# Performance work log

Measured on AMD Instinct MI355X. Metric: run time of the kernel, lower is better.

## Reference

```python
import jax, jax.numpy as jnp
import numpy as np

RADIUS = 1.3
COARSE = 32          # coarse_reso
FINE = 2             # fine_reso[0]
NUM_ATOMS = 32
SH_DIM = 9           # (sh_deg+1)^2, sh_deg=2
DATA_DIM = SH_DIM * 3 + 1  # 28
BATCH = 512
N_INT = COARSE * 3 * 2 * FINE  # 384 intersections per ray

# 8 trilinear neighbor offsets, same order as the torch module
_OFFSETS = jnp.array([[-1, -1, -1], [-1, -1, 1], [-1, 1, -1], [-1, 1, 1],
                      [1, -1, -1], [1, -1, 1], [1, 1, -1], [1, 1, 1]], dtype=jnp.float32)


def sh_encode(d):
    """Real spherical harmonics basis, degree 2 (9 components), on normalized dirs."""
    d = d / jnp.linalg.norm(d, axis=-1, keepdims=True)
    x, y, z = d[..., 0], d[..., 1], d[..., 2]
    c0 = 0.28209479177387814
    c1 = 0.48860251190291987
    c2a = 1.0925484305920792
    c2b = 0.31539156525252005
    c2c = 0.5462742152960396
    return jnp.stack([
        c0 * jnp.ones_like(x),
        -c1 * y, c1 * z, -c1 * x,
        c2a * x * y, -c2a * y * z,
        c2b * (2.0 * z * z - x * x - y * y),
        -c2a * x * z,
        c2c * (x * x - y * y)], axis=-1)


def dict_interp(pts, grid, atoms):
    """Multi-res voxel trilinear gather + dictionary-atom accumulate.
    pts: [N,3] world coords; grid: [COARSE^3, A]; atoms: [FINE^3, A, D]."""
    fine_vlen = (2.0 * RADIUS / COARSE) / FINE
    p = (pts + RADIUS) / fine_vlen                       # [N,3] fine-grid coords
    pre = p[:, None, :] + _OFFSETS[None] / 2.0           # [N,8,3]
    post = jnp.clip(jnp.floor(pre), 0.0, COARSE * FINE - 1)
    offs = jnp.abs(p[:, None, :] - (post + 0.5))         # [N,8,3]
    w = jnp.prod(1.0 - offs, axis=-1)                    # [N,8] trilinear weights
    idx = post.astype(jnp.int32)
    c = idx // FINE                                      # coarse cell per-axis
    f = idx % FINE                                       # fine cell per-axis
    cflat = (c[..., 0] * COARSE + c[..., 1]) * COARSE + c[..., 2]  # [N,8]
    fflat = (f[..., 0] * FINE + f[..., 1]) * FINE + f[..., 2]      # [N,8]
    out = jnp.zeros((pts.shape[0], DATA_DIM), pts.dtype)
    for n in range(8):
        cv = grid[cflat[:, n]]                           # [N,A] gathered coarse weights
        av = atoms[fflat[:, n]]                          # [N,A,D] gathered atoms
        out = out + w[:, n, None] * jnp.einsum('na,nad->nd', cv, av)
    return out


def setup_inputs() -> dict:
    key = jax.random.key(0)
    k1, k2, k3, k4 = jax.random.split(key, 4)
    rays_o = jax.random.uniform(k1, (BATCH, 3), jnp.float32, -0.5, 0.5)
    rays_d = jax.random.normal(k2, (BATCH, 3), jnp.float32)
    rays_d = rays_d / jnp.linalg.norm(rays_d, axis=-1, keepdims=True)
    grid = 0.01 * jax.random.normal(k3, (COARSE ** 3, NUM_ATOMS), jnp.float32)
    atoms = jnp.concatenate([
        jax.random.uniform(k4, (FINE ** 3, NUM_ATOMS, DATA_DIM - 1), jnp.float32),
        jnp.full((FINE ** 3, NUM_ATOMS, 1), 0.01, jnp.float32)], axis=-1)
    return {"rays_o": rays_o, "rays_d": rays_d, "grid": grid, "atoms": atoms, "grid_id": 0}


def reference(rays_o, rays_d, grid, atoms, grid_id):
    del grid_id  # single scene
    step = ((2.0 * RADIUS / COARSE) / FINE) / 2.0
    # sample_proposal (no_grad in the original)
    off_pos = (RADIUS - rays_o) / rays_d
    off_neg = (-RADIUS - rays_o) / rays_d
    start = jnp.max(jnp.minimum(off_pos, off_neg), axis=-1, keepdims=True)
    steps = jnp.arange(N_INT, dtype=rays_o.dtype)[None]
    intersections = jax.lax.stop_gradient(start + steps * step)  # [B, N_INT]
    ts = intersections[:, :-1]                                    # [B, S]
    pts = jax.lax.stop_gradient(
        rays_o[:, None, :] + ts[..., None] * rays_d[:, None, :])  # [B,S,3]
    mask = jnp.all((pts > -RADIUS) & (pts < RADIUS), axis=-1)     # [B,S]
    B, S = ts.shape
    data = dict_interp(pts.reshape(-1, 3), grid, atoms).reshape(B, S, DATA_DIM)
    # masked_scatter_ equivalent: zero out out-of-box samples
    sigma = jnp.where(mask, jax.nn.relu(data[..., -1]), 0.0)
    dists = (intersections[:, 1:] - intersections[:, :-1]) * jnp.linalg.norm(rays_d, axis=-1, keepdims=True)
    alpha = 1.0 - jnp.exp(-sigma * dists)
    T = jnp.cumprod(1.0 - alpha + 1e-10, axis=-1)
    T = jnp.concatenate([jnp.ones_like(T[:, :1]), T[:, :-1]], axis=-1)
    abs_light = alpha * T                                         # [B,S]
    sh = sh_encode(rays_d)                                        # [B,SH_DIM]
    sh_vals = data[..., :-1].reshape(B, S, 3, SH_DIM)
    rgb_s = jnp.einsum('bk,bsck->bsc', sh, sh_vals)               # [B,S,3]
    rgb_s = jnp.where(mask[..., None], rgb_s, 0.0)
    rgb = jnp.sum(abs_light[..., None] * jax.nn.sigmoid(rgb_s), axis=1)
    rgb = rgb + (1.0 - jnp.sum(abs_light, axis=-1, keepdims=True))  # white background
    depth = jnp.sum(abs_light * ts, axis=-1)
    consistency_loss = jnp.zeros((), rgb.dtype)  # noise_std == 0
    return rgb, alpha, depth, consistency_loss
```

## Files before the change

### kernel.cpp

```cpp
#include <hip/hip_runtime.h>
#include <math.h>

#define R_ 1.3f
#define NCOARSE 32
#define SAMPLES 383
#define BATCH 512
#define STEPSZ 0.0203125f
#define INV_FINE_VLEN 24.615384615384617f

using f32x4 = __attribute__((ext_vector_type(4))) float;
using s16x8 = __attribute__((ext_vector_type(8))) short;
using u32x4 = __attribute__((ext_vector_type(4))) unsigned int;

__device__ __forceinline__ unsigned int packbf2(float lo, float hi) {
    unsigned int a = __builtin_bit_cast(unsigned int, lo);
    unsigned int b = __builtin_bit_cast(unsigned int, hi);
    a = (a + 0x7fffu + ((a >> 16) & 1u)) >> 16;
    b = (b + 0x7fffu + ((b >> 16) & 1u)) >> 16;
    return (a & 0xffffu) | (b << 16);
}

__device__ __forceinline__ void dimwc(float p, float* W, int* C) {
    float post0 = fminf(fmaxf(floorf(p - 0.5f), 0.f), 63.f);
    float post1 = fminf(fmaxf(floorf(p + 0.5f), 0.f), 63.f);
    float w0 = 1.f - fabsf(p - (post0 + 0.5f));
    float w1 = 1.f - fabsf(p - (post1 + 0.5f));
    int i0 = (int)post0, i1 = (int)post1;
    int f0 = i0 & 1, f1 = i1 & 1;
    W[0] = (f0 == 0 ? w0 : 0.f) + (f1 == 0 ? w1 : 0.f);
    W[1] = (f0 == 1 ? w0 : 0.f) + (f1 == 1 ? w1 : 0.f);
    int c0 = i0 >> 1, c1 = i1 >> 1;
    C[0] = (f0 == 0) ? c0 : c1;
    C[1] = (f0 == 1) ? c0 : c1;
}

__global__ __launch_bounds__(512, 4) void dp_fused(
    const float* __restrict__ rays_o, const float* __restrict__ rays_d,
    const float* __restrict__ grid, const float* __restrict__ atoms,
    float* __restrict__ out_rgb, float* __restrict__ out_alpha,
    float* __restrict__ out_depth, float* __restrict__ out_loss)
{
    __shared__ u32x4 Bf[16][64];
    __shared__ u32x4 Abuf[8][256];
    __shared__ float alpha_l[384];
    __shared__ float sig_l[384][3];

    const int b = blockIdx.x;
    const int tid = threadIdx.x;
    const int wid = tid >> 6, l = tid & 63;
    const int sl = l & 15, fp = l >> 4;
    if (b == 0 && tid == 0) out_loss[0] = 0.f;

    if (tid < 384) alpha_l[tid] = 0.f;
    {
        float* sf = &sig_l[0][0];
        for (int i = tid; i < 384 * 3; i += 512) sf[i] = 0.f;
    }

    for (int sidx = tid; sidx < 1024; sidx += 512) {
        const int ll = sidx & 63, nt = (sidx >> 6) & 1, kb = sidx >> 7;
        const int a0 = (ll >> 4) * 8, d = nt * 16 + (ll & 15);
        u32x4 o = {0u, 0u, 0u, 0u};
        if (d < 28) {
#pragma unroll
            for (int e2 = 0; e2 < 4; ++e2) {
                const float lo = atoms[(kb * 32 + a0 + 2 * e2) * 28 + d];
                const float hi = atoms[(kb * 32 + a0 + 2 * e2 + 1) * 28 + d];
                o[e2] = packbf2(lo, hi);
            }
        }
        Bf[sidx >> 6][ll] = o;
    }

    const float ox = rays_o[3 * b], oy = rays_o[3 * b + 1], oz = rays_o[3 * b + 2];
    const float dx = rays_d[3 * b], dy = rays_d[3 * b + 1], dz = rays_d[3 * b + 2];
    const float start = fmaxf(fmaxf(
        fminf((R_ - ox) / dx, (-R_ - ox) / dx),
        fminf((R_ - oy) / dy, (-R_ - oy) / dy)),
        fminf((R_ - oz) / dz, (-R_ - oz) / dz));
    const float t_exit = fminf(fminf(
        fmaxf((R_ - ox) / dx, (-R_ - ox) / dx),
        fmaxf((R_ - oy) / dy, (-R_ - oy) / dy)),
        fmaxf((R_ - oz) / dz, (-R_ - oz) / dz));
    const int ns = (int)floorf((t_exit - start) / STEPSZ) + 2;
    const int ntiles = min(24, (ns >> 4) + 2);

    const float lend = sqrtf(dx * dx + dy * dy + dz * dz);
    const float dist = STEPSZ * lend;
    const float inv = 1.f / lend;
    const float nx = dx * inv, ny = dy * inv, nz = dz * inv;
    float sh[9];
    sh[0] = 0.28209479177387814f;
    sh[1] = -0.48860251190291987f * ny;
    sh[2] = 0.48860251190291987f * nz;
    sh[3] = -0.48860251190291987f * nx;
    sh[4] = 1.0925484305920792f * nx * ny;
    sh[5] = -1.0925484305920792f * ny * nz;
    sh[6] = 0.31539156525252005f * (2.f * nz * nz - nx * nx - ny * ny);
    sh[7] = -1.0925484305920792f * nx * nz;
    sh[8] = 0.5462742152960396f * (nx * nx - ny * ny);

    __syncthreads();

    u32x4* W4 = &Abuf[wid][0];
    float* Dbuf = (float*)W4;

    for (int t = wid; t < ntiles; t += 8) {
        const int s = t * 16 + sl;
        const float tt = start + s * STEPSZ;
        const float px = ox + tt * dx, py = oy + tt * dy, pz = oz + tt * dz;
        const bool m = (s < SAMPLES) &&
                       (px > -R_ && px < R_ && py > -R_ && py < R_ && pz > -R_ && pz < R_);
        if (__ballot(m) == 0ull) continue;

        float W0[2], W1[2], W2[2];
        int C0[2], C1[2], C2[2];
        dimwc((px + R_) * INV_FINE_VLEN, W0, C0);
        dimwc((py + R_) * INV_FINE_VLEN, W1, C1);
        dimwc((pz + R_) * INV_FINE_VLEN, W2, C2);
        const float msk = m ? 1.f : 0.f;

        f32x4 acc0 = {0.f, 0.f, 0.f, 0.f};
        f32x4 acc1 = {0.f, 0.f, 0.f, 0.f};
#pragma unroll
        for (int stg = 0; stg < 2; ++stg) {
            const int f = 4 * stg + fp;
            const int fx = (f >> 2) & 1, fy = (f >> 1) & 1, fz = f & 1;
            const float wf = msk * W0[fx] * W1[fy] * W2[fz];
            const int cf = (C0[fx] * NCOARSE + C1[fy]) * NCOARSE + C2[fz];
            const f32x4* gr = (const f32x4*)(grid + cf * 32);
#pragma unroll
            for (int g4 = 0; g4 < 4; ++g4) {
                const f32x4 v0 = gr[2 * g4];
                const f32x4 v1 = gr[2 * g4 + 1];
                u32x4 o;
                o.x = packbf2(wf * v0.x, wf * v0.y);
                o.y = packbf2(wf * v0.z, wf * v0.w);
                o.z = packbf2(wf * v1.x, wf * v1.y);
                o.w = packbf2(wf * v1.z, wf * v1.w);
                W4[fp * 64 + 16 * g4 + sl] = o;
            }
#pragma unroll
            for (int kb2 = 0; kb2 < 4; ++kb2) {
                const int kb = 4 * stg + kb2;
                const s16x8 af = __builtin_bit_cast(s16x8, W4[kb2 * 64 + l]);
                acc0 = __builtin_amdgcn_mfma_f32_16x16x32_bf16(
                    af, __builtin_bit_cast(s16x8, Bf[kb * 2 + 0][l]), acc0, 0, 0, 0);
                acc1 = __builtin_amdgcn_mfma_f32_16x16x32_bf16(
                    af, __builtin_bit_cast(s16x8, Bf[kb * 2 + 1][l]), acc1, 0, 0, 0);
            }
        }

#pragma unroll
        for (int r = 0; r < 4; ++r) {
            Dbuf[(4 * fp + r) * 33 + sl]      = acc0[r];
            Dbuf[(4 * fp + r) * 33 + sl + 16] = acc1[r];
        }

        const int s2 = l >> 2, c = l & 3;
        const int so = t * 16 + s2;
        if (c == 3) {
            const float sigma = fmaxf(Dbuf[s2 * 33 + 27], 0.f);
            alpha_l[so] = 1.f - expf(-sigma * dist);
        } else {
            float r_ = 0.f;
#pragma unroll
            for (int k = 0; k < 9; ++k) r_ += sh[k] * Dbuf[s2 * 33 + c * 9 + k];
            sig_l[so][c] = 1.f / (1.f + expf(-r_));
        }
    }

    __syncthreads();

    if (tid < SAMPLES) out_alpha[b * SAMPLES + tid] = alpha_l[tid];

    if (wid == 0) {
        float Tacc = 1.f;
        float r0 = 0.f, r1 = 0.f, r2 = 0.f, sd = 0.f, sa = 0.f;
        for (int j = 0; j < 6; ++j) {
            const int s = j * 64 + l;
            const bool v = s < SAMPLES;
            const float a = v ? alpha_l[s] : 0.f;
            float incl = v ? (1.f - a + 1e-10f) : 1.f;
#pragma unroll
            for (int off = 1; off < 64; off <<= 1) {
                const float tm = __shfl_up(incl, off, 64);
                if (l >= off) incl *= tm;
            }
            float excl = __shfl_up(incl, 1, 64);
            if (l == 0) excl = 1.f;
            const float T = Tacc * excl;
            const float al = a * T;
            if (v) {
                r0 += al * sig_l[s][0];
                r1 += al * sig_l[s][1];
                r2 += al * sig_l[s][2];
                sd += al * (start + s * STEPSZ);
                sa += al;
            }
            Tacc *= __shfl(incl, 63, 64);
        }
#pragma unroll
        for (int m = 32; m > 0; m >>= 1) {
            r0 += __shfl_xor(r0, m, 64);
            r1 += __shfl_xor(r1, m, 64);
            r2 += __shfl_xor(r2, m, 64);
            sd += __shfl_xor(sd, m, 64);
            sa += __shfl_xor(sa, m, 64);
        }
        if (l == 0) {
            const float base = 1.f - sa;
            out_rgb[b * 3 + 0] = r0 + base;
            out_rgb[b * 3 + 1] = r1 + base;
            out_rgb[b * 3 + 2] = r2 + base;
            out_depth[b] = sd;
        }
    }
}

extern "C" void kernel_launch(void* const* d_in, const int* in_sizes, int n_in,
                              void* d_out, int out_size, void* d_ws, size_t ws_size,
                              hipStream_t stream) {
    const float* rays_o = (const float*)d_in[0];
    const float* rays_d = (const float*)d_in[1];
    const float* grid   = (const float*)d_in[2];
    const float* atoms  = (const float*)d_in[3];
    float* out   = (float*)d_out;
    float* rgb   = out;
    float* alpha = out + BATCH * 3;
    float* depth = out + BATCH * 3 + BATCH * SAMPLES;
    float* loss  = out + BATCH * 3 + BATCH * SAMPLES + BATCH;

    dp_fused<<<dim3(BATCH), dim3(512), 0, stream>>>(
        rays_o, rays_d, grid, atoms, rgb, alpha, depth, loss);
}
```

Before: 16.53 us.

## Prefetch grid/atom loads, use hardware bf16 cast, parallelize transmittance scan across warps

After: 17.27 us. 4.5% more time.

```diff
diff --git a/kernel.cpp b/kernel.cpp
--- a/kernel.cpp
+++ b/kernel.cpp
@@ -11,13 +11,13 @@
 using f32x4 = __attribute__((ext_vector_type(4))) float;
 using s16x8 = __attribute__((ext_vector_type(8))) short;
 using u32x4 = __attribute__((ext_vector_type(4))) unsigned int;
+using bf16x2 = __attribute__((ext_vector_type(2))) __bf16;
 
 __device__ __forceinline__ unsigned int packbf2(float lo, float hi) {
-    unsigned int a = __builtin_bit_cast(unsigned int, lo);
-    unsigned int b = __builtin_bit_cast(unsigned int, hi);
-    a = (a + 0x7fffu + ((a >> 16) & 1u)) >> 16;
-    b = (b + 0x7fffu + ((b >> 16) & 1u)) >> 16;
-    return (a & 0xffffu) | (b << 16);
+    bf16x2 v;
+    v.x = (__bf16)lo;
+    v.y = (__bf16)hi;
+    return __builtin_bit_cast(unsigned int, v);
 }
 
 __device__ __forceinline__ void dimwc(float p, float* W, int* C) {
@@ -44,32 +44,32 @@
     __shared__ u32x4 Abuf[8][256];
     __shared__ float alpha_l[384];
     __shared__ float sig_l[384][3];
+    __shared__ float segtot[8];
+    __shared__ float part[6][5];
 
     const int b = blockIdx.x;
     const int tid = threadIdx.x;
     const int wid = tid >> 6, l = tid & 63;
     const int sl = l & 15, fp = l >> 4;
+
+    const int s0i = tid, s1i = tid + 512;
+    const int ll0 = s0i & 63, nt0 = (s0i >> 6) & 1, kb0 = s0i >> 7;
+    const int ll1 = s1i & 63, nt1 = (s1i >> 6) & 1, kb1 = s1i >> 7;
+    const int a00 = (ll0 >> 4) * 8, d0 = nt0 * 16 + (ll0 & 15);
+    const int a01 = (ll1 >> 4) * 8, d1 = nt1 * 16 + (ll1 & 15);
+    float la0[8], la1[8];
+#pragma unroll
+    for (int j = 0; j < 8; ++j) {
+        la0[j] = (d0 < 28) ? atoms[(kb0 * 32 + a00 + j) * 28 + d0] : 0.f;
+        la1[j] = (d1 < 28) ? atoms[(kb1 * 32 + a01 + j) * 28 + d1] : 0.f;
+    }
+
     if (b == 0 && tid == 0) out_loss[0] = 0.f;
 
     if (tid < 384) alpha_l[tid] = 0.f;
     {
         float* sf = &sig_l[0][0];
         for (int i = tid; i < 384 * 3; i += 512) sf[i] = 0.f;
-    }
-
-    for (int sidx = tid; sidx < 1024; sidx += 512) {
-        const int ll = sidx & 63, nt = (sidx >> 6) & 1, kb = sidx >> 7;
-        const int a0 = (ll >> 4) * 8, d = nt * 16 + (ll & 15);
-        u32x4 o = {0u, 0u, 0u, 0u};
-        if (d < 28) {
-#pragma unroll
-            for (int e2 = 0; e2 < 4; ++e2) {
-                const float lo = atoms[(kb * 32 + a0 + 2 * e2) * 28 + d];
-                const float hi = atoms[(kb * 32 + a0 + 2 * e2 + 1) * 28 + d];
-                o[e2] = packbf2(lo, hi);
-            }
-        }
-        Bf[sidx >> 6][ll] = o;
     }
 
     const float ox = rays_o[3 * b], oy = rays_o[3 * b + 1], oz = rays_o[3 * b + 2];
@@ -100,6 +100,17 @@
     sh[7] = -1.0925484305920792f * nx * nz;
     sh[8] = 0.5462742152960396f * (nx * nx - ny * ny);
 
+    {
+        u32x4 o0, o1;
+#pragma unroll
+        for (int e2 = 0; e2 < 4; ++e2) {
+            o0[e2] = packbf2(la0[2 * e2], la0[2 * e2 + 1]);
+            o1[e2] = packbf2(la1[2 * e2], la1[2 * e2 + 1]);
+        }
+        Bf[s0i >> 6][ll0] = o0;
+        Bf[s1i >> 6][ll1] = o1;
+    }
+
     __syncthreads();
 
     u32x4* W4 = &Abuf[wid][0];
@@ -120,35 +131,69 @@
         dimwc((pz + R_) * INV_FINE_VLEN, W2, C2);
         const float msk = m ? 1.f : 0.f;
 
+        const int f0c = fp, f1c = 4 + fp;
+        const float wf0 = msk * W0[(f0c >> 2) & 1] * W1[(f0c >> 1) & 1] * W2[f0c & 1];
+        const float wf1 = msk * W0[(f1c >> 2) & 1] * W1[(f1c >> 1) & 1] * W2[f1c & 1];
+        const int cf0 = (C0[(f0c >> 2) & 1] * NCOARSE + C1[(f0c >> 1) & 1]) * NCOARSE + C2[f0c & 1];
+        const int cf1 = (C0[(f1c >> 2) & 1] * NCOARSE + C1[(f1c >> 1) & 1]) * NCOARSE + C2[f1c & 1];
+        const f32x4* gr0 = (const f32x4*)(grid + cf0 * 32);
+        const f32x4* gr1 = (const f32x4*)(grid + cf1 * 32);
+
+        f32x4 q0 = gr1[0], q1 = gr1[1], q2 = gr1[2], q3 = gr1[3];
+        f32x4 q4 = gr1[4], q5 = gr1[5], q6 = gr1[6], q7 = gr1[7];
+
         f32x4 acc0 = {0.f, 0.f, 0.f, 0.f};
         f32x4 acc1 = {0.f, 0.f, 0.f, 0.f};
-#pragma unroll
-        for (int stg = 0; stg < 2; ++stg) {
-            const int f = 4 * stg + fp;
-            const int fx = (f >> 2) & 1, fy = (f >> 1) & 1, fz = f & 1;
-            const float wf = msk * W0[fx] * W1[fy] * W2[fz];
-            const int cf = (C0[fx] * NCOARSE + C1[fy]) * NCOARSE + C2[fz];
-            const f32x4* gr = (const f32x4*)(grid + cf * 32);
-#pragma unroll
-            for (int g4 = 0; g4 < 4; ++g4) {
-                const f32x4 v0 = gr[2 * g4];
-                const f32x4 v1 = gr[2 * g4 + 1];
-                u32x4 o;
-                o.x = packbf2(wf * v0.x, wf * v0.y);
-                o.y = packbf2(wf * v0.z, wf * v0.w);
-                o.z = packbf2(wf * v1.x, wf * v1.y);
-                o.w = packbf2(wf * v1.z, wf * v1.w);
-                W4[fp * 64 + 16 * g4 + sl] = o;
-            }
-#pragma unroll
-            for (int kb2 = 0; kb2 < 4; ++kb2) {
-                const int kb = 4 * stg + kb2;
-                const s16x8 af = __builtin_bit_cast(s16x8, W4[kb2 * 64 + l]);
-                acc0 = __builtin_amdgcn_mfma_f32_16x16x32_bf16(
-                    af, __builtin_bit_cast(s16x8, Bf[kb * 2 + 0][l]), acc0, 0, 0, 0);
-                acc1 = __builtin_amdgcn_mfma_f32_16x16x32_bf16(
-                    af, __builtin_bit_cast(s16x8, Bf[kb * 2 + 1][l]), acc1, 0, 0, 0);
-            }
+
+#pragma unroll
+        for (int g4 = 0; g4 < 4; ++g4) {
+            const f32x4 v0 = gr0[2 * g4];
+            const f32x4 v1 = gr0[2 * g4 + 1];
+            u32x4 o;
+            o.x = packbf2(wf0 * v0.x, wf0 * v0.y);
+            o.y = packbf2(wf0 * v0.z, wf0 * v0.w);
+            o.z = packbf2(wf0 * v1.x, wf0 * v1.y);
+            o.w = packbf2(wf0 * v1.z, wf0 * v1.w);
+            W4[fp * 64 + 16 * g4 + sl] = o;
+        }
+#pragma unroll
+        for (int kb2 = 0; kb2 < 4; ++kb2) {
+            const s16x8 af = __builtin_bit_cast(s16x8, W4[kb2 * 64 + l]);
+            acc0 = __builtin_amdgcn_mfma_f32_16x16x32_bf16(
+                af, __builtin_bit_cast(s16x8, Bf[kb2 * 2 + 0][l]), acc0, 0, 0, 0);
+            acc1 = __builtin_amdgcn_mfma_f32_16x16x32_bf16(
+                af, __builtin_bit_cast(s16x8, Bf[kb2 * 2 + 1][l]), acc1, 0, 0, 0);
+        }
+        {
+            u32x4 o;
+            o.x = packbf2(wf1 * q0.x, wf1 * q0.y);
+            o.y = packbf2(wf1 * q0.z, wf1 * q0.w);
+            o.z = packbf2(wf1 * q1.x, wf1 * q1.y);
+            o.w = packbf2(wf1 * q1.z, wf1 * q1.w);
+            W4[fp * 64 + sl] = o;
+            o.x = packbf2(wf1 * q2.x, wf1 * q2.y);
+            o.y = packbf2(wf1 * q2.z, wf1 * q2.w);
+            o.z = packbf2(wf1 * q3.x, wf1 * q3.y);
+            o.w = packbf2(wf1 * q3.z, wf1 * q3.w);
+            W4[fp * 64 + 16 + sl] = o;
+            o.x = packbf2(wf1 * q4.x, wf1 * q4.y);
+            o.y = packbf2(wf1 * q4.z, wf1 * q4.w);
+            o.z = packbf2(wf1 * q5.x, wf1 * q5.y);
+            o.w = packbf2(wf1 * q5.z, wf1 * q5.w);
+            W4[fp * 64 + 32 + sl] = o;
+            o.x = packbf2(wf1 * q6.x, wf1 * q6.y);
+            o.y = packbf2(wf1 * q6.z, wf1 * q6.w);
+            o.z = packbf2(wf1 * q7.x, wf1 * q7.y);
+            o.w = packbf2(wf1 * q7.z, wf1 * q7.w);
+            W4[fp * 64 + 48 + sl] = o;
+        }
+#pragma unroll
+        for (int kb2 = 0; kb2 < 4; ++kb2) {
+            const s16x8 af = __builtin_bit_cast(s16x8, W4[kb2 * 64 + l]);
+            acc0 = __builtin_amdgcn_mfma_f32_16x16x32_bf16(
+                af, __builtin_bit_cast(s16x8, Bf[(4 + kb2) * 2 + 0][l]), acc0, 0, 0, 0);
+            acc1 = __builtin_amdgcn_mfma_f32_16x16x32_bf16(
+                af, __builtin_bit_cast(s16x8, Bf[(4 + kb2) * 2 + 1][l]), acc1, 0, 0, 0);
         }
 
 #pragma unroll
@@ -161,12 +206,12 @@
         const int so = t * 16 + s2;
         if (c == 3) {
             const float sigma = fmaxf(Dbuf[s2 * 33 + 27], 0.f);
-            alpha_l[so] = 1.f - expf(-sigma * dist);
+            alpha_l[so] = 1.f - __expf(-sigma * dist);
         } else {
             float r_ = 0.f;
 #pragma unroll
             for (int k = 0; k < 9; ++k) r_ += sh[k] * Dbuf[s2 * 33 + c * 9 + k];
-            sig_l[so][c] = 1.f / (1.f + expf(-r_));
+            sig_l[so][c] = __builtin_amdgcn_rcpf(1.f + __expf(-r_));
         }
     }
 
@@ -174,47 +219,59 @@
 
     if (tid < SAMPLES) out_alpha[b * SAMPLES + tid] = alpha_l[tid];
 
-    if (wid == 0) {
-        float Tacc = 1.f;
+    float a_s = 0.f, incl = 1.f;
+    if (wid < 6) {
+        const int s = wid * 64 + l;
+        const bool v = s < SAMPLES;
+        a_s = v ? alpha_l[s] : 0.f;
+        incl = v ? (1.f - a_s + 1e-10f) : 1.f;
+#pragma unroll
+        for (int off = 1; off < 64; off <<= 1) {
+            const float tm = __shfl_up(incl, off, 64);
+            if (l >= off) incl *= tm;
+        }
+        if (l == 63) segtot[wid] = incl;
+    }
+    __syncthreads();
+    if (wid < 6) {
+        float pre = 1.f;
+        for (int k = 0; k < wid; ++k) pre *= segtot[k];
+        float excl = __shfl_up(incl, 1, 64);
+        if (l == 0) excl = 1.f;
+        const int s = wid * 64 + l;
+        const bool v = s < SAMPLES;
+        const float al = v ? a_s * pre * excl : 0.f;
+        float r0 = al * sig_l[s][0];
+        float r1 = al * sig_l[s][1];
+        float r2 = al * sig_l[s][2];
+        float sd = al * (start + s * STEPSZ);
+        float sa = al;
+#pragma unroll
+        for (int m2 = 32; m2 > 0; m2 >>= 1) {
+            r0 += __shfl_xor(r0, m2, 64);
+            r1 += __shfl_xor(r1, m2, 64);
+            r2 += __shfl_xor(r2, m2, 64);
+            sd += __shfl_xor(sd, m2, 64);
+            sa += __shfl_xor(sa, m2, 64);
+        }
+        if (l == 0) {
+            part[wid][0] = r0; part[wid][1] = r1; part[wid][2] = r2;
+            part[wid][3] = sd; part[wid][4] = sa;
+        }
+    }
+    __syncthreads();
+    if (tid == 0) {
         float r0 = 0.f, r1 = 0.f, r2 = 0.f, sd = 0.f, sa = 0.f;
+#pragma unroll
         for (int j = 0; j < 6; ++j) {
-            const int s = j * 64 + l;
-            const bool v = s < SAMPLES;
-            const float a = v ? alpha_l[s] : 0.f;
-            float incl = v ? (1.f - a + 1e-10f) : 1.f;
-#pragma unroll
-            for (int off = 1; off < 64; off <<= 1) {
-                const float tm = __shfl_up(incl, off, 64);
-                if (l >= off) incl *= tm;
-            }
-            float excl = __shfl_up(incl, 1, 64);
-            if (l == 0) excl = 1.f;
-            const float T = Tacc * excl;
-            const float al = a * T;
-            if (v) {
-                r0 += al * sig_l[s][0];
-                r1 += al * sig_l[s][1];
-                r2 += al * sig_l[s][2];
-                sd += al * (start + s * STEPSZ);
-                sa += al;
-            }
-            Tacc *= __shfl(incl, 63, 64);
-        }
-#pragma unroll
-        for (int m = 32; m > 0; m >>= 1) {
-            r0 += __shfl_xor(r0, m, 64);
-            r1 += __shfl_xor(r1, m, 64);
-            r2 += __shfl_xor(r2, m, 64);
-            sd += __shfl_xor(sd, m, 64);
-            sa += __shfl_xor(sa, m, 64);
-        }
-        if (l == 0) {
-            const float base = 1.f - sa;
-            out_rgb[b * 3 + 0] = r0 + base;
-            out_rgb[b * 3 + 1] = r1 + base;
-            out_rgb[b * 3 + 2] = r2 + base;
-            out_depth[b] = sd;
-        }
+            r0 += part[j][0]; r1 += part[j][1]; r2 += part[j][2];
+            sd += part[j][3]; sa += part[j][4];
+        }
+        const float base = 1.f - sa;
+        out_rgb[b * 3 + 0] = r0 + base;
+        out_rgb[b * 3 + 1] = r1 + base;
+        out_rgb[b * 3 + 2] = r2 + base;
+        out_depth[b] = sd;
     }
 }
 
```
